# Performance work log

Measured on AMD Instinct MI355X. Metric: run time of the kernel, lower is better.

Reference implementation:

```python
import jax, jax.numpy as jnp
import numpy as np

TYPE_PANEL, TYPE_DIALOG, TYPE_CHAR = 1, 2, 3
NUM_ELEMS = 64  # max element index per type (panel count cap per page)
B, S, D = 8, 4096, 768
NPC, NDS = 4, 4  # num_panel_classes, num_dialog_shapes


def setup_inputs() -> dict:
    key = jax.random.key(0)
    ks = jax.random.split(key, 16)
    w = lambda k, shp: jax.random.normal(k, shp, dtype=jnp.float32) * 0.02
    return {
        "element_types": jax.random.randint(ks[0], (B, S), 0, 4, dtype=jnp.int32),
        "element_indices": jax.random.randint(ks[1], (B, S), 0, NUM_ELEMS, dtype=jnp.int32),
        "parent_panel_indices": jax.random.randint(ks[2], (B, S), 0, NUM_ELEMS, dtype=jnp.int32),
        "style_vector": jax.random.normal(ks[3], (B, 4), dtype=jnp.float32),
        "type_emb": w(ks[4], (4, D)),
        "index_emb": w(ks[5], (NUM_ELEMS, D)),
        "parent_emb": w(ks[6], (NUM_ELEMS, D)),
        "style_w": w(ks[7], (4, D)),
        "style_b": jnp.zeros((D,), jnp.float32),
        "ln_g": jnp.ones((D,), jnp.float32),
        "ln_b": jnp.zeros((D,), jnp.float32),
        "panel_w": w(ks[8], (D, NPC + 4)),
        "panel_b": jnp.zeros((NPC + 4,), jnp.float32),
        "dialog_w": w(ks[9], (2 * D, NDS + 4)),
        "dialog_b": jnp.zeros((NDS + 4,), jnp.float32),
        "char_w": w(ks[10], (2 * D, 4)),
        "char_b": jnp.zeros((4,), jnp.float32),
    }


def reference(element_types, element_indices, parent_panel_indices, style_vector,
              type_emb, index_emb, parent_emb, style_w, style_b, ln_g, ln_b,
              panel_w, panel_b, dialog_w, dialog_b, char_w, char_b):
    Bv, Sv = element_types.shape
    # --- TokenLayoutEncoder: embedding sum + style projection + LayerNorm ---
    x = type_emb[element_types] + index_emb[element_indices] + parent_emb[parent_panel_indices]
    x = x + (style_vector @ style_w + style_b)[:, None, :]
    mu = x.mean(-1, keepdims=True)
    var = ((x - mu) ** 2).mean(-1, keepdims=True)
    feats = (x - mu) * jax.lax.rsqrt(var + 1e-5) * ln_g + ln_b  # (B,S,D)

    # --- vectorized _build_parent_remap: orig panel idx -> kept panel order pos ---
    panel_mask = element_types == TYPE_PANEL                      # (B,S)
    kept = (jnp.cumsum(panel_mask, axis=1) - 1).astype(jnp.int32) # order pos of each panel token
    brow = jnp.arange(Bv, dtype=jnp.int32)[:, None]
    col = jnp.where(panel_mask, element_indices, NUM_ELEMS)       # dummy slot for non-panels
    remap = (jnp.full((Bv, NUM_ELEMS + 1), -1, jnp.int32)
             .at[brow, col].max(kept))[:, :NUM_ELEMS]             # (B, NUM_ELEMS)
    # kept panel order pos -> sequence position (for parent feature gather)
    slot = jnp.where(panel_mask, kept, Sv)
    seq_ids = jnp.broadcast_to(jnp.arange(Sv, dtype=jnp.int32), (Bv, Sv))
    pos_table = (jnp.zeros((Bv, Sv + 1), jnp.int32)
                 .at[brow, slot].set(seq_ids))[:, :Sv]            # (B,S)

    # --- parent_pos per token (DIALOG/CHAR only), -1 otherwise ---
    child_mask = (element_types == TYPE_DIALOG) | (element_types == TYPE_CHAR)
    ppos = jnp.where(child_mask,
                     jnp.take_along_axis(remap, parent_panel_indices, axis=1), -1)
    valid = ppos >= 0
    pseq = jnp.take_along_axis(pos_table, jnp.clip(ppos, 0, Sv - 1), axis=1)
    parent_feats = jnp.take_along_axis(feats, pseq[..., None], axis=1)
    parent_feats = parent_feats * valid[..., None].astype(feats.dtype)
    cat = jnp.concatenate([feats, parent_feats], axis=-1)         # (B,S,2D)

    # --- ParallelPredictionHeads, masked per token type ---
    panel_out = (feats @ panel_w + panel_b) * panel_mask[..., None].astype(feats.dtype)
    dmask = ((element_types == TYPE_DIALOG) & valid)[..., None].astype(feats.dtype)
    cmask = ((element_types == TYPE_CHAR) & valid)[..., None].astype(feats.dtype)
    dialog_out = (cat @ dialog_w + dialog_b) * dmask
    char_out = (cat @ char_w + char_b) * cmask
    return panel_out, dialog_out, char_out
```

## Files before the change

### kernel.cpp

```cpp
#include <hip/hip_runtime.h>

#define NB 8
#define NS 4096
#define ND 768
#define NT 32768

typedef float4 f4;
typedef __attribute__((ext_vector_type(8))) short short8;
typedef __attribute__((ext_vector_type(4))) float floatx4;
typedef unsigned short ushort_t;
typedef unsigned int uint_t;

static __device__ __forceinline__ ushort_t f2b(float f) {
    union { float f; uint_t u; } v; v.f = f;
    uint_t r = (v.u + 0x7FFFu + ((v.u >> 16) & 1u)) >> 16;
    return (ushort_t)r;
}
static __device__ __forceinline__ float b2f(ushort_t s) {
    union { uint_t u; float f; } v; v.u = ((uint_t)s) << 16;
    return v.f;
}
static __device__ __forceinline__ f4 ld4(const float* p) { return *(const f4*)p; }

__global__ __launch_bounds__(256) void k1(
    const int* __restrict__ et, const int* __restrict__ ei,
    const float* __restrict__ sv, const float* __restrict__ sw,
    const float* __restrict__ sb,
    int* __restrict__ table, float* __restrict__ sprj, float* __restrict__ out)
{
    const int tid = blockIdx.x * 256 + threadIdx.x;
    for (int i = tid; i < 163840; i += 33280)
        ((f4*)out)[i] = make_float4(0.f, 0.f, 0.f, 0.f);

    if (blockIdx.x < 128) {
        if (et[tid] == 1)
            atomicMax(&table[(tid >> 12) * 64 + ei[tid]], tid & (NS - 1));
    } else {
        const int lane = threadIdx.x & 63;
        const int b = (blockIdx.x - 128) * 4 + (threadIdx.x >> 6);
        const float s0 = sv[b*4+0], s1 = sv[b*4+1], s2 = sv[b*4+2], s3 = sv[b*4+3];
        #pragma unroll
        for (int g = 0; g < 3; ++g) {
            int i = g*64 + lane;
            f4 w0 = ((const f4*)sw)[i],       w1 = ((const f4*)sw)[192+i];
            f4 w2 = ((const f4*)sw)[384+i],   w3 = ((const f4*)sw)[576+i];
            f4 bb = ((const f4*)sb)[i];
            f4 r;
            r.x = bb.x + s0*w0.x + s1*w1.x + s2*w2.x + s3*w3.x;
            r.y = bb.y + s0*w0.y + s1*w1.y + s2*w2.y + s3*w3.y;
            r.z = bb.z + s0*w0.z + s1*w1.z + s2*w2.z + s3*w3.z;
            r.w = bb.w + s0*w0.w + s1*w1.w + s2*w2.w + s3*w3.w;
            ((f4*)(sprj + b*ND))[i] = r;
        }
    }
}

__global__ __launch_bounds__(256) void k2(
    const int* __restrict__ et, const int* __restrict__ ei, const int* __restrict__ ppi,
    const float* __restrict__ temb, const float* __restrict__ iemb,
    const float* __restrict__ pemb, const float* __restrict__ lng,
    const float* __restrict__ lnb,
    const int* __restrict__ table, const float* __restrict__ sprj,
    ushort_t* __restrict__ pfeat, int* __restrict__ cnt, int* __restrict__ lists)
{
    if (blockIdx.x < 128) {
        const int lane = threadIdx.x & 63;
        const int slot = blockIdx.x * 4 + (threadIdx.x >> 6);
        const int pp = table[slot];
        if (pp < 0) return;
        const int b = slot >> 6;
        const int ptok = b * NS + pp;
        const float* ie = iemb + ei[ptok] * ND;
        const float* pe = pemb + ppi[ptok] * ND;
        const float* sp = sprj + b * ND;

        f4 x[3]; float s1 = 0.f;
        #pragma unroll
        for (int g = 0; g < 3; ++g) {
            int i = g*64 + lane;
            f4 a = ((const f4*)(temb + ND))[i], c = ((const f4*)ie)[i];
            f4 d = ((const f4*)pe)[i],          s = ((const f4*)sp)[i];
            x[g].x = a.x + c.x + d.x + s.x;
            x[g].y = a.y + c.y + d.y + s.y;
            x[g].z = a.z + c.z + d.z + s.z;
            x[g].w = a.w + c.w + d.w + s.w;
            s1 += x[g].x + x[g].y + x[g].z + x[g].w;
        }
        #pragma unroll
        for (int o = 1; o < 64; o <<= 1) s1 += __shfl_xor(s1, o, 64);
        float mu = s1 * (1.f/ND);
        float s2 = 0.f;
        #pragma unroll
        for (int g = 0; g < 3; ++g) {
            float dx = x[g].x-mu, dy = x[g].y-mu, dz = x[g].z-mu, dw_ = x[g].w-mu;
            s2 += dx*dx + dy*dy + dz*dz + dw_*dw_;
        }
        #pragma unroll
        for (int o = 1; o < 64; o <<= 1) s2 += __shfl_xor(s2, o, 64);
        float rs = rsqrtf(s2 * (1.f/ND) + 1e-5f);
        ushort_t* dst = pfeat + (size_t)slot * ND;
        #pragma unroll
        for (int g = 0; g < 3; ++g) {
            int i = g*64 + lane;
            f4 gg = ((const f4*)lng)[i], bb = ((const f4*)lnb)[i];
            ushort_t r0 = f2b((x[g].x-mu)*rs*gg.x + bb.x);
            ushort_t r1 = f2b((x[g].y-mu)*rs*gg.y + bb.y);
            ushort_t r2 = f2b((x[g].z-mu)*rs*gg.z + bb.z);
            ushort_t r3 = f2b((x[g].w-mu)*rs*gg.w + bb.w);
            *(uint2*)(dst + 4*i) = make_uint2((uint_t)r0 | ((uint_t)r1 << 16),
                                              (uint_t)r2 | ((uint_t)r3 << 16));
        }
    } else {
        const int t = (blockIdx.x - 128) * 256 + threadIdx.x;
        const int lane = threadIdx.x & 63;
        const int ty = et[t];
        const bool vld = (ty >= 2) && (table[(t >> 12) * 64 + ppi[t]] >= 0);
        #pragma unroll
        for (int i = 1; i <= 3; ++i) {
            bool p = (i == 1) ? (ty == 1) : (ty == i && vld);
            unsigned long long mask = __ballot(p);
            if (mask == 0ull) continue;
            int leader = __ffsll((long long)mask) - 1;
            int base = 0;
            if (lane == leader)
                base = atomicAdd(&cnt[i - 1], __popcll(mask));
            base = __shfl(base, leader, 64);
            if (p) {
                int prefix = __popcll(mask & ((1ull << lane) - 1ull));
                lists[(i - 1) * NT + base + prefix] = t;
            }
        }
    }
}

__global__ __launch_bounds__(256) void k3(
    const int* __restrict__ ei, const int* __restrict__ ppi,
    const float* __restrict__ temb, const float* __restrict__ iemb,
    const float* __restrict__ pemb, const float* __restrict__ lng,
    const float* __restrict__ lnb,
    const float* __restrict__ pw, const float* __restrict__ pb,
    const float* __restrict__ dw, const float* __restrict__ db,
    const float* __restrict__ cw, const float* __restrict__ cb,
    const float* __restrict__ sprj, const ushort_t* __restrict__ pfeat,
    const int* __restrict__ cnt, const int* __restrict__ lists,
    float* __restrict__ out)
{
    __shared__ uint4 bbuf[48 * 64];
    const int ty = (blockIdx.x >> 9) + 1;
    const int chunk = blockIdx.x & 511;
    const int cn = cnt[ty - 1];
    if (chunk * 64 >= cn) return;

    const int W = (ty == 3) ? 4 : 8;
    const int wsh = (ty == 3) ? 2 : 3;
    const int Ktot = (ty == 1) ? 768 : 1536;
    const float* wsrc = (ty == 1) ? pw : (ty == 2) ? dw : cw;
    const float* bias = (ty == 1) ? pb : (ty == 2) ? db : cb;
    const int* list = lists + (ty - 1) * NT;

    const int nq = (Ktot / 32) * 64;
    for (int i = threadIdx.x; i < nq; i += 256)
        bbuf[i] = make_uint4(0u, 0u, 0u, 0u);
    __syncthreads();
    {
        const int f4n = (Ktot * W) / 4;
        for (int i = threadIdx.x; i < f4n; i += 256) {
            f4 v = ((const f4*)wsrc)[i];
            #pragma unroll
            for (int q = 0; q < 4; ++q) {
                int e = 4*i + q;
                int k = e >> wsh, n = e & (W - 1);
                int l = (((k >> 3) & 3) << 4) + n;
                int s = k >> 5, j = k & 7;
                float val = (q == 0) ? v.x : (q == 1) ? v.y : (q == 2) ? v.z : v.w;
                ((ushort_t*)bbuf)[(s*64 + l)*8 + j] = f2b(val);
            }
        }
    }
    __syncthreads();

    const int lane = threadIdx.x & 63;
    const int gbase = chunk * 64 + (threadIdx.x >> 6) * 16;
    if (gbase >= cn) return;
    const int m = lane & 15;
    const int koff = (lane >> 4) * 8;
    const int slot = min(gbase + m, cn - 1);
    const int tl = list[slot];
    const int b = tl >> 12;
    const int eidx = ei[tl], pidx = ppi[tl];
    const float* ie_p = iemb + eidx * ND;
    const float* pe_p = pemb + pidx * ND;
    const float* sp_p = sprj + b * ND;
    const float* te_p = temb + ty * ND;

    short8 xf[24];
    float sum = 0.f, sq = 0.f;
    #pragma unroll
    for (int s = 0; s < 24; ++s) {
        int d0 = 32*s + koff;
        f4 a0 = ld4(te_p + d0), a1 = ld4(te_p + d0 + 4);
        f4 c0 = ld4(ie_p + d0), c1 = ld4(ie_p + d0 + 4);
        f4 e0 = ld4(pe_p + d0), e1 = ld4(pe_p + d0 + 4);
        f4 p0 = ld4(sp_p + d0), p1 = ld4(sp_p + d0 + 4);
        float x0 = a0.x + c0.x + e0.x + p0.x;
        float x1 = a0.y + c0.y + e0.y + p0.y;
        float x2 = a0.z + c0.z + e0.z + p0.z;
        float x3 = a0.w + c0.w + e0.w + p0.w;
        float x4 = a1.x + c1.x + e1.x + p1.x;
        float x5 = a1.y + c1.y + e1.y + p1.y;
        float x6 = a1.z + c1.z + e1.z + p1.z;
        float x7 = a1.w + c1.w + e1.w + p1.w;
        sum += (x0+x1)+(x2+x3)+(x4+x5)+(x6+x7);
        sq  += (x0*x0+x1*x1)+(x2*x2+x3*x3)+(x4*x4+x5*x5)+(x6*x6+x7*x7);
        short8 t8;
        t8[0]=(short)f2b(x0); t8[1]=(short)f2b(x1); t8[2]=(short)f2b(x2); t8[3]=(short)f2b(x3);
        t8[4]=(short)f2b(x4); t8[5]=(short)f2b(x5); t8[6]=(short)f2b(x6); t8[7]=(short)f2b(x7);
        xf[s] = t8;
    }
    sum += __shfl_xor(sum, 16, 64); sum += __shfl_xor(sum, 32, 64);
    sq  += __shfl_xor(sq , 16, 64); sq  += __shfl_xor(sq , 32, 64);
    float mu = sum * (1.f/ND);
    float rs = rsqrtf(sq * (1.f/ND) - mu*mu + 1e-5f);

    floatx4 acc = {0.f, 0.f, 0.f, 0.f};
    #pragma unroll
    for (int s = 0; s < 24; ++s) {
        int d0 = 32*s + koff;
        f4 g0 = ld4(lng + d0), g1 = ld4(lng + d0 + 4);
        f4 h0 = ld4(lnb + d0), h1 = ld4(lnb + d0 + 4);
        short8 ff;
        ff[0] = (short)f2b((b2f((ushort_t)xf[s][0]) - mu)*rs*g0.x + h0.x);
        ff[1] = (short)f2b((b2f((ushort_t)xf[s][1]) - mu)*rs*g0.y + h0.y);
        ff[2] = (short)f2b((b2f((ushort_t)xf[s][2]) - mu)*rs*g0.z + h0.z);
        ff[3] = (short)f2b((b2f((ushort_t)xf[s][3]) - mu)*rs*g0.w + h0.w);
        ff[4] = (short)f2b((b2f((ushort_t)xf[s][4]) - mu)*rs*g1.x + h1.x);
        ff[5] = (short)f2b((b2f((ushort_t)xf[s][5]) - mu)*rs*g1.y + h1.y);
        ff[6] = (short)f2b((b2f((ushort_t)xf[s][6]) - mu)*rs*g1.z + h1.z);
        ff[7] = (short)f2b((b2f((ushort_t)xf[s][7]) - mu)*rs*g1.w + h1.w);
        short8 bf = ((short8*)bbuf)[s*64 + lane];
        acc = __builtin_amdgcn_mfma_f32_16x16x32_bf16(ff, bf, acc, 0, 0, 0);
    }
    if (ty != 1) {
        const ushort_t* pf_p = pfeat + (size_t)(b*64 + pidx) * ND;
        #pragma unroll
        for (int s = 0; s < 24; ++s) {
            short8 af = *(const short8*)(pf_p + 32*s + koff);
            short8 bf = ((short8*)bbuf)[(24 + s)*64 + lane];
            acc = __builtin_amdgcn_mfma_f32_16x16x32_bf16(af, bf, acc, 0, 0, 0);
        }
    }

    const int n = lane & 15;
    const float bv = (n < W) ? bias[n] : 0.f;
    const long obase = (ty == 1) ? 0L : (ty == 2) ? (long)NT*8 : (long)NT*16;
    #pragma unroll
    for (int r = 0; r < 4; ++r) {
        int row = (lane >> 4) * 4 + r;
        int rslot = gbase + row;
        if (n < W && rslot < cn) {
            int tr = list[rslot];
            out[obase + (long)tr * W + n] = acc[r] + bv;
        }
    }
}

extern "C" void kernel_launch(void* const* d_in, const int* in_sizes, int n_in,
                              void* d_out, int out_size, void* d_ws, size_t ws_size,
                              hipStream_t stream) {
    const int* et  = (const int*)d_in[0];
    const int* ei  = (const int*)d_in[1];
    const int* ppi = (const int*)d_in[2];
    const float* sv   = (const float*)d_in[3];
    const float* temb = (const float*)d_in[4];
    const float* iemb = (const float*)d_in[5];
    const float* pemb = (const float*)d_in[6];
    const float* sw   = (const float*)d_in[7];
    const float* sb   = (const float*)d_in[8];
    const float* lng  = (const float*)d_in[9];
    const float* lnb  = (const float*)d_in[10];
    const float* pw   = (const float*)d_in[11];
    const float* pb   = (const float*)d_in[12];
    const float* dw   = (const float*)d_in[13];
    const float* db   = (const float*)d_in[14];
    const float* cw   = (const float*)d_in[15];
    const float* cbp  = (const float*)d_in[16];
    float* out = (float*)d_out;

    int*      table = (int*)d_ws;
    int*      cnt   = (int*)((char*)d_ws + 2048);
    float*    sprj  = (float*)((char*)d_ws + 4096);
    ushort_t* pfeat = (ushort_t*)((char*)d_ws + 28672);
    int*      lists = (int*)((char*)d_ws + 815104);

    hipMemsetAsync(table, 0xFF, 512 * sizeof(int), stream);
    hipMemsetAsync(cnt, 0x00, 3 * sizeof(int), stream);

    k1<<<130, 256, 0, stream>>>(et, ei, sv, sw, sb, table, sprj, out);
    k2<<<256, 256, 0, stream>>>(et, ei, ppi, temb, iemb, pemb, lng, lnb,
                                table, sprj, pfeat, cnt, lists);
    k3<<<1536, 256, 0, stream>>>(ei, ppi, temb, iemb, pemb, lng, lnb,
                                 pw, pb, dw, db, cw, cbp, sprj, pfeat,
                                 cnt, lists, out);
}
```

Measured before the change: 157.0 us.

## Fold LayerNorm affine into head weights and pre-swizzle weights once

The LayerNorm gamma is folded into the head weights, and gamma/beta correction terms are precomputed. The LN normalization is then applied after the MFMA as rs*(acc - mu*colsum) + beta-term. This removes the second pass over cached bf16 activations and the per-block LDS weight swizzle. Type embedding and style projection are merged into one combined bias table per type and batch, and the cnt memset is folded into k1. The risk is extra bf16 rounding error, because unnormalized x is quantized and the mean is subtracted afterwards, which can cancel badly.

```diff
diff --git a/kernel.cpp b/kernel.cpp
--- a/kernel.cpp
+++ b/kernel.cpp
@@ -16,51 +16,109 @@
     uint_t r = (v.u + 0x7FFFu + ((v.u >> 16) & 1u)) >> 16;
     return (ushort_t)r;
 }
-static __device__ __forceinline__ float b2f(ushort_t s) {
-    union { uint_t u; float f; } v; v.u = ((uint_t)s) << 16;
-    return v.f;
-}
 static __device__ __forceinline__ f4 ld4(const float* p) { return *(const f4*)p; }
+
+static __device__ __forceinline__ float wred(float v) {
+    v += __shfl_xor(v, 32, 64);
+    v += __shfl_xor(v, 16, 64);
+    v += __shfl_xor(v, 8, 64);
+    v += __shfl_xor(v, 4, 64);
+    v += __shfl_xor(v, 2, 64);
+    v += __shfl_xor(v, 1, 64);
+    return v;
+}
 
 __global__ __launch_bounds__(256) void k1(
     const int* __restrict__ et, const int* __restrict__ ei,
     const float* __restrict__ sv, const float* __restrict__ sw,
-    const float* __restrict__ sb,
-    int* __restrict__ table, float* __restrict__ sprj, float* __restrict__ out)
+    const float* __restrict__ sb, const float* __restrict__ temb,
+    const float* __restrict__ lng, const float* __restrict__ lnb,
+    const float* __restrict__ pw, const float* __restrict__ dw,
+    const float* __restrict__ cw,
+    int* __restrict__ table, int* __restrict__ cnt, float* __restrict__ cors,
+    float* __restrict__ comb, uint4* __restrict__ Bswz, float* __restrict__ out)
 {
-    const int tid = blockIdx.x * 256 + threadIdx.x;
-    for (int i = tid; i < 163840; i += 33280)
-        ((f4*)out)[i] = make_float4(0.f, 0.f, 0.f, 0.f);
-
-    if (blockIdx.x < 128) {
-        if (et[tid] == 1)
-            atomicMax(&table[(tid >> 12) * 64 + ei[tid]], tid & (NS - 1));
-    } else {
-        const int lane = threadIdx.x & 63;
-        const int b = (blockIdx.x - 128) * 4 + (threadIdx.x >> 6);
+    const int blk = blockIdx.x, tid = threadIdx.x;
+    if (blk < 128) {
+        const int t = blk * 256 + tid;
+        for (int i = t; i < 163840; i += 32768)
+            ((f4*)out)[i] = make_float4(0.f, 0.f, 0.f, 0.f);
+        if (blk == 0 && tid < 3) cnt[tid] = 0;
+        if (et[t] == 1)
+            atomicMax(&table[(t >> 12) * 64 + ei[t]], t & (NS - 1));
+    } else if (blk < 134) {
+        const int lane = tid & 63;
+        const int idx = (blk - 128) * 4 + (tid >> 6);
+        const int ty = 1 + (idx >> 3), b = idx & 7;
         const float s0 = sv[b*4+0], s1 = sv[b*4+1], s2 = sv[b*4+2], s3 = sv[b*4+3];
         #pragma unroll
         for (int g = 0; g < 3; ++g) {
             int i = g*64 + lane;
-            f4 w0 = ((const f4*)sw)[i],       w1 = ((const f4*)sw)[192+i];
-            f4 w2 = ((const f4*)sw)[384+i],   w3 = ((const f4*)sw)[576+i];
+            f4 w0 = ((const f4*)sw)[i],     w1 = ((const f4*)sw)[192+i];
+            f4 w2 = ((const f4*)sw)[384+i], w3 = ((const f4*)sw)[576+i];
             f4 bb = ((const f4*)sb)[i];
+            f4 te = ((const f4*)(temb + ty*ND))[i];
             f4 r;
-            r.x = bb.x + s0*w0.x + s1*w1.x + s2*w2.x + s3*w3.x;
-            r.y = bb.y + s0*w0.y + s1*w1.y + s2*w2.y + s3*w3.y;
-            r.z = bb.z + s0*w0.z + s1*w1.z + s2*w2.z + s3*w3.z;
-            r.w = bb.w + s0*w0.w + s1*w1.w + s2*w2.w + s3*w3.w;
-            ((f4*)(sprj + b*ND))[i] = r;
-        }
+            r.x = te.x + bb.x + s0*w0.x + s1*w1.x + s2*w2.x + s3*w3.x;
+            r.y = te.y + bb.y + s0*w0.y + s1*w1.y + s2*w2.y + s3*w3.y;
+            r.z = te.z + bb.z + s0*w0.z + s1*w1.z + s2*w2.z + s3*w3.z;
+            r.w = te.w + bb.w + s0*w0.w + s1*w1.w + s2*w2.w + s3*w3.w;
+            ((f4*)(comb + idx*ND))[i] = r;
+        }
+    } else if (blk == 134) {
+        const int lane = tid & 63;
+        const int h = tid >> 6;
+        if (h < 3) {
+            const int W = (h == 2) ? 4 : 8;
+            const float* wsrc = (h == 0) ? pw : (h == 1) ? dw : cw;
+            for (int n = 0; n < 16; ++n) {
+                float a1 = 0.f, a2 = 0.f;
+                if (n < W) {
+                    for (int i = 0; i < 12; ++i) {
+                        int k = i*64 + lane;
+                        float wv = wsrc[k*W + n];
+                        a1 += lng[k] * wv;
+                        a2 += lnb[k] * wv;
+                    }
+                }
+                a1 = wred(a1); a2 = wred(a2);
+                if (lane == 0) { cors[h*16 + n] = a1; cors[48 + h*16 + n] = a2; }
+            }
+        }
+    } else {
+        const int e = (blk - 135) * 256 + tid;
+        const int h = (e < 1536) ? 0 : (e < 4608) ? 1 : 2;
+        const int base = (h == 0) ? 0 : (h == 1) ? 1536 : 4608;
+        const int idx = e - base;
+        const int s = idx >> 6, l = idx & 63;
+        const int n = l & 15, kq = l >> 4;
+        const int W = (h == 2) ? 4 : 8;
+        const float* wsrc = (h == 0) ? pw : (h == 1) ? dw : cw;
+        ushort_t v[8];
+        #pragma unroll
+        for (int j = 0; j < 8; ++j) {
+            int k = 32*s + 8*kq + j;
+            float val = 0.f;
+            if (n < W) {
+                float sc = (k < 768) ? lng[k] : 1.f;
+                val = wsrc[k*W + n] * sc;
+            }
+            v[j] = f2b(val);
+        }
+        uint4 q;
+        q.x = (uint_t)v[0] | ((uint_t)v[1] << 16);
+        q.y = (uint_t)v[2] | ((uint_t)v[3] << 16);
+        q.z = (uint_t)v[4] | ((uint_t)v[5] << 16);
+        q.w = (uint_t)v[6] | ((uint_t)v[7] << 16);
+        Bswz[e] = q;
     }
 }
 
 __global__ __launch_bounds__(256) void k2(
     const int* __restrict__ et, const int* __restrict__ ei, const int* __restrict__ ppi,
-    const float* __restrict__ temb, const float* __restrict__ iemb,
-    const float* __restrict__ pemb, const float* __restrict__ lng,
-    const float* __restrict__ lnb,
-    const int* __restrict__ table, const float* __restrict__ sprj,
+    const float* __restrict__ iemb, const float* __restrict__ pemb,
+    const float* __restrict__ lng, const float* __restrict__ lnb,
+    const int* __restrict__ table, const float* __restrict__ comb,
     ushort_t* __restrict__ pfeat, int* __restrict__ cnt, int* __restrict__ lists)
 {
     if (blockIdx.x < 128) {
@@ -72,32 +130,27 @@
         const int ptok = b * NS + pp;
         const float* ie = iemb + ei[ptok] * ND;
         const float* pe = pemb + ppi[ptok] * ND;
-        const float* sp = sprj + b * ND;
+        const float* cm = comb + b * ND;
 
         f4 x[3]; float s1 = 0.f;
         #pragma unroll
         for (int g = 0; g < 3; ++g) {
             int i = g*64 + lane;
-            f4 a = ((const f4*)(temb + ND))[i], c = ((const f4*)ie)[i];
-            f4 d = ((const f4*)pe)[i],          s = ((const f4*)sp)[i];
-            x[g].x = a.x + c.x + d.x + s.x;
-            x[g].y = a.y + c.y + d.y + s.y;
-            x[g].z = a.z + c.z + d.z + s.z;
-            x[g].w = a.w + c.w + d.w + s.w;
+            f4 a = ((const f4*)cm)[i], c = ((const f4*)ie)[i], d = ((const f4*)pe)[i];
+            x[g].x = a.x + c.x + d.x;
+            x[g].y = a.y + c.y + d.y;
+            x[g].z = a.z + c.z + d.z;
+            x[g].w = a.w + c.w + d.w;
             s1 += x[g].x + x[g].y + x[g].z + x[g].w;
         }
-        #pragma unroll
-        for (int o = 1; o < 64; o <<= 1) s1 += __shfl_xor(s1, o, 64);
-        float mu = s1 * (1.f/ND);
+        float mu = wred(s1) * (1.f/ND);
         float s2 = 0.f;
         #pragma unroll
         for (int g = 0; g < 3; ++g) {
             float dx = x[g].x-mu, dy = x[g].y-mu, dz = x[g].z-mu, dw_ = x[g].w-mu;
             s2 += dx*dx + dy*dy + dz*dz + dw_*dw_;
         }
-        #pragma unroll
-        for (int o = 1; o < 64; o <<= 1) s2 += __shfl_xor(s2, o, 64);
-        float rs = rsqrtf(s2 * (1.f/ND) + 1e-5f);
+        float rs = rsqrtf(wred(s2) * (1.f/ND) + 1e-5f);
         ushort_t* dst = pfeat + (size_t)slot * ND;
         #pragma unroll
         for (int g = 0; g < 3; ++g) {
@@ -135,131 +188,84 @@
 
 __global__ __launch_bounds__(256) void k3(
     const int* __restrict__ ei, const int* __restrict__ ppi,
-    const float* __restrict__ temb, const float* __restrict__ iemb,
-    const float* __restrict__ pemb, const float* __restrict__ lng,
-    const float* __restrict__ lnb,
-    const float* __restrict__ pw, const float* __restrict__ pb,
-    const float* __restrict__ dw, const float* __restrict__ db,
-    const float* __restrict__ cw, const float* __restrict__ cb,
-    const float* __restrict__ sprj, const ushort_t* __restrict__ pfeat,
+    const float* __restrict__ iemb, const float* __restrict__ pemb,
+    const float* __restrict__ pb, const float* __restrict__ db,
+    const float* __restrict__ cb,
+    const float* __restrict__ comb, const ushort_t* __restrict__ pfeat,
+    const float* __restrict__ cors, const uint4* __restrict__ Bswz,
     const int* __restrict__ cnt, const int* __restrict__ lists,
     float* __restrict__ out)
 {
-    __shared__ uint4 bbuf[48 * 64];
     const int ty = (blockIdx.x >> 9) + 1;
     const int chunk = blockIdx.x & 511;
     const int cn = cnt[ty - 1];
     if (chunk * 64 >= cn) return;
-
-    const int W = (ty == 3) ? 4 : 8;
-    const int wsh = (ty == 3) ? 2 : 3;
-    const int Ktot = (ty == 1) ? 768 : 1536;
-    const float* wsrc = (ty == 1) ? pw : (ty == 2) ? dw : cw;
-    const float* bias = (ty == 1) ? pb : (ty == 2) ? db : cb;
-    const int* list = lists + (ty - 1) * NT;
-
-    const int nq = (Ktot / 32) * 64;
-    for (int i = threadIdx.x; i < nq; i += 256)
-        bbuf[i] = make_uint4(0u, 0u, 0u, 0u);
-    __syncthreads();
-    {
-        const int f4n = (Ktot * W) / 4;
-        for (int i = threadIdx.x; i < f4n; i += 256) {
-            f4 v = ((const f4*)wsrc)[i];
-            #pragma unroll
-            for (int q = 0; q < 4; ++q) {
-                int e = 4*i + q;
-                int k = e >> wsh, n = e & (W - 1);
-                int l = (((k >> 3) & 3) << 4) + n;
-                int s = k >> 5, j = k & 7;
-                float val = (q == 0) ? v.x : (q == 1) ? v.y : (q == 2) ? v.z : v.w;
-                ((ushort_t*)bbuf)[(s*64 + l)*8 + j] = f2b(val);
-            }
-        }
-    }
-    __syncthreads();
-
     const int lane = threadIdx.x & 63;
     const int gbase = chunk * 64 + (threadIdx.x >> 6) * 16;
     if (gbase >= cn) return;
+
+    const int W = (ty == 3) ? 4 : 8;
+    const float* bias = (ty == 1) ? pb : (ty == 2) ? db : cb;
+    const uint4* bsw = Bswz + ((ty == 1) ? 0 : (ty == 2) ? 1536 : 4608);
+    const int* list = lists + (ty - 1) * NT;
+
     const int m = lane & 15;
-    const int koff = (lane >> 4) * 8;
+    const int kq = lane >> 4;
+    const int koff = kq * 8;
     const int slot = min(gbase + m, cn - 1);
     const int tl = list[slot];
     const int b = tl >> 12;
-    const int eidx = ei[tl], pidx = ppi[tl];
-    const float* ie_p = iemb + eidx * ND;
+    const int pidx = ppi[tl];
+    const float* cm_p = comb + ((ty - 1) * 8 + b) * ND;
+    const float* ie_p = iemb + ei[tl] * ND;
     const float* pe_p = pemb + pidx * ND;
-    const float* sp_p = sprj + b * ND;
-    const float* te_p = temb + ty * ND;
-
-    short8 xf[24];
+    const ushort_t* pf_p = pfeat + (size_t)(b * 64 + pidx) * ND;
+
+    floatx4 accO = {0.f, 0.f, 0.f, 0.f};
+    floatx4 accP = {0.f, 0.f, 0.f, 0.f};
     float sum = 0.f, sq = 0.f;
     #pragma unroll
     for (int s = 0; s < 24; ++s) {
-        int d0 = 32*s + koff;
-        f4 a0 = ld4(te_p + d0), a1 = ld4(te_p + d0 + 4);
-        f4 c0 = ld4(ie_p + d0), c1 = ld4(ie_p + d0 + 4);
-        f4 e0 = ld4(pe_p + d0), e1 = ld4(pe_p + d0 + 4);
-        f4 p0 = ld4(sp_p + d0), p1 = ld4(sp_p + d0 + 4);
-        float x0 = a0.x + c0.x + e0.x + p0.x;
-        float x1 = a0.y + c0.y + e0.y + p0.y;
-        float x2 = a0.z + c0.z + e0.z + p0.z;
-        float x3 = a0.w + c0.w + e0.w + p0.w;
-        float x4 = a1.x + c1.x + e1.x + p1.x;
-        float x5 = a1.y + c1.y + e1.y + p1.y;
-        float x6 = a1.z + c1.z + e1.z + p1.z;
-        float x7 = a1.w + c1.w + e1.w + p1.w;
+        const int d0 = 32*s + koff;
+        f4 c0 = ld4(cm_p + d0), c1 = ld4(cm_p + d0 + 4);
+        f4 i0 = ld4(ie_p + d0), i1 = ld4(ie_p + d0 + 4);
+        f4 p0 = ld4(pe_p + d0), p1 = ld4(pe_p + d0 + 4);
+        float x0 = c0.x + i0.x + p0.x, x1 = c0.y + i0.y + p0.y;
+        float x2 = c0.z + i0.z + p0.z, x3 = c0.w + i0.w + p0.w;
+        float x4 = c1.x + i1.x + p1.x, x5 = c1.y + i1.y + p1.y;
+        float x6 = c1.z + i1.z + p1.z, x7 = c1.w + i1.w + p1.w;
         sum += (x0+x1)+(x2+x3)+(x4+x5)+(x6+x7);
         sq  += (x0*x0+x1*x1)+(x2*x2+x3*x3)+(x4*x4+x5*x5)+(x6*x6+x7*x7);
-        short8 t8;
-        t8[0]=(short)f2b(x0); t8[1]=(short)f2b(x1); t8[2]=(short)f2b(x2); t8[3]=(short)f2b(x3);
-        t8[4]=(short)f2b(x4); t8[5]=(short)f2b(x5); t8[6]=(short)f2b(x6); t8[7]=(short)f2b(x7);
-        xf[s] = t8;
+        short8 a;
+        a[0]=(short)f2b(x0); a[1]=(short)f2b(x1); a[2]=(short)f2b(x2); a[3]=(short)f2b(x3);
+        a[4]=(short)f2b(x4); a[5]=(short)f2b(x5); a[6]=(short)f2b(x6); a[7]=(short)f2b(x7);
+        short8 bO = *(const short8*)&bsw[s*64 + lane];
+        accO = __builtin_amdgcn_mfma_f32_16x16x32_bf16(a, bO, accO, 0, 0, 0);
+        if (ty != 1) {
+            short8 aP = *(const short8*)(pf_p + 32*s + koff);
+            short8 bP = *(const short8*)&bsw[(24 + s)*64 + lane];
+            accP = __builtin_amdgcn_mfma_f32_16x16x32_bf16(aP, bP, accP, 0, 0, 0);
+        }
     }
     sum += __shfl_xor(sum, 16, 64); sum += __shfl_xor(sum, 32, 64);
     sq  += __shfl_xor(sq , 16, 64); sq  += __shfl_xor(sq , 32, 64);
-    float mu = sum * (1.f/ND);
-    float rs = rsqrtf(sq * (1.f/ND) - mu*mu + 1e-5f);
-
-    floatx4 acc = {0.f, 0.f, 0.f, 0.f};
-    #pragma unroll
-    for (int s = 0; s < 24; ++s) {
-        int d0 = 32*s + koff;
-        f4 g0 = ld4(lng + d0), g1 = ld4(lng + d0 + 4);
-        f4 h0 = ld4(lnb + d0), h1 = ld4(lnb + d0 + 4);
-        short8 ff;
-        ff[0] = (short)f2b((b2f((ushort_t)xf[s][0]) - mu)*rs*g0.x + h0.x);
-        ff[1] = (short)f2b((b2f((ushort_t)xf[s][1]) - mu)*rs*g0.y + h0.y);
-        ff[2] = (short)f2b((b2f((ushort_t)xf[s][2]) - mu)*rs*g0.z + h0.z);
-        ff[3] = (short)f2b((b2f((ushort_t)xf[s][3]) - mu)*rs*g0.w + h0.w);
-        ff[4] = (short)f2b((b2f((ushort_t)xf[s][4]) - mu)*rs*g1.x + h1.x);
-        ff[5] = (short)f2b((b2f((ushort_t)xf[s][5]) - mu)*rs*g1.y + h1.y);
-        ff[6] = (short)f2b((b2f((ushort_t)xf[s][6]) - mu)*rs*g1.z + h1.z);
-        ff[7] = (short)f2b((b2f((ushort_t)xf[s][7]) - mu)*rs*g1.w + h1.w);
-        short8 bf = ((short8*)bbuf)[s*64 + lane];
-        acc = __builtin_amdgcn_mfma_f32_16x16x32_bf16(ff, bf, acc, 0, 0, 0);
-    }
-    if (ty != 1) {
-        const ushort_t* pf_p = pfeat + (size_t)(b*64 + pidx) * ND;
-        #pragma unroll
-        for (int s = 0; s < 24; ++s) {
-            short8 af = *(const short8*)(pf_p + 32*s + koff);
-            short8 bf = ((short8*)bbuf)[(24 + s)*64 + lane];
-            acc = __builtin_amdgcn_mfma_f32_16x16x32_bf16(af, bf, acc, 0, 0, 0);
-        }
-    }
+    const float mu = sum * (1.f/ND);
+    const float rs = rsqrtf(sq * (1.f/ND) - mu*mu + 1e-5f);
 
     const int n = lane & 15;
-    const float bv = (n < W) ? bias[n] : 0.f;
+    const float co1 = cors[(ty-1)*16 + n];
+    const float co2 = cors[48 + (ty-1)*16 + n];
+    const float bv  = (n < W) ? bias[n] : 0.f;
     const long obase = (ty == 1) ? 0L : (ty == 2) ? (long)NT*8 : (long)NT*16;
     #pragma unroll
     for (int r = 0; r < 4; ++r) {
-        int row = (lane >> 4) * 4 + r;
-        int rslot = gbase + row;
+        const int row = kq*4 + r;
+        const float mur = __shfl(mu, row, 64);
+        const float rsr = __shfl(rs, row, 64);
+        const int rslot = gbase + row;
         if (n < W && rslot < cn) {
             int tr = list[rslot];
-            out[obase + (long)tr * W + n] = acc[r] + bv;
+            out[obase + (long)tr * W + n] = rsr*(accO[r] - mur*co1) + co2 + accP[r] + bv;
         }
     }
 }
@@ -288,17 +294,18 @@
 
     int*      table = (int*)d_ws;
     int*      cnt   = (int*)((char*)d_ws + 2048);
-    float*    sprj  = (float*)((char*)d_ws + 4096);
-    ushort_t* pfeat = (ushort_t*)((char*)d_ws + 28672);
-    int*      lists = (int*)((char*)d_ws + 815104);
+    float*    cors  = (float*)((char*)d_ws + 2304);
+    float*    comb  = (float*)((char*)d_ws + 4096);
+    ushort_t* pfeat = (ushort_t*)((char*)d_ws + 81920);
+    int*      lists = (int*)((char*)d_ws + 868352);
+    uint4*    Bswz  = (uint4*)((char*)d_ws + 1261568);
 
     hipMemsetAsync(table, 0xFF, 512 * sizeof(int), stream);
-    hipMemsetAsync(cnt, 0x00, 3 * sizeof(int), stream);
-
-    k1<<<130, 256, 0, stream>>>(et, ei, sv, sw, sb, table, sprj, out);
-    k2<<<256, 256, 0, stream>>>(et, ei, ppi, temb, iemb, pemb, lng, lnb,
-                                table, sprj, pfeat, cnt, lists);
-    k3<<<1536, 256, 0, stream>>>(ei, ppi, temb, iemb, pemb, lng, lnb,
-                                 pw, pb, dw, db, cw, cbp, sprj, pfeat,
-                                 cnt, lists, out);
-}
+
+    k1<<<165, 256, 0, stream>>>(et, ei, sv, sw, sb, temb, lng, lnb,
+                                pw, dw, cw, table, cnt, cors, comb, Bswz, out);
+    k2<<<256, 256, 0, stream>>>(et, ei, ppi, iemb, pemb, lng, lnb,
+                                table, comb, pfeat, cnt, lists);
+    k3<<<1536, 256, 0, stream>>>(ei, ppi, iemb, pemb, pb, db, cbp,
+                                 comb, pfeat, cors, Bswz, cnt, lists, out);
+}
```

Result: no change. 155.2 us (-1.2%).
